# Optimization experiments

Hardware: AMD Instinct MI355X
Metric: run time of the kernel (lower is better)

## Reference

```python
import jax, jax.numpy as jnp
import numpy as np

VOCAB = 32000
WORDVEC = 256
HIDDEN = 512
NULL_TOKEN = 0


def setup_inputs() -> dict:
    key = jax.random.key(0)
    ks = jax.random.split(key, 8)
    N, Tp1 = 16, 257
    captions = jax.random.randint(ks[0], (N, Tp1), 0, VOCAB, dtype=jnp.int64 if jax.config.jax_enable_x64 else jnp.int32)
    W_embed = jax.random.normal(ks[1], (VOCAB, WORDVEC), jnp.float32) / 100.0
    Wx = jax.random.normal(ks[2], (WORDVEC, 4 * HIDDEN), jnp.float32) / np.sqrt(WORDVEC).astype(np.float32)
    Wh = jax.random.normal(ks[3], (HIDDEN, 4 * HIDDEN), jnp.float32) / np.sqrt(HIDDEN).astype(np.float32)
    b = jnp.zeros((4 * HIDDEN,), jnp.float32)
    W_vocab = jax.random.normal(ks[4], (HIDDEN, VOCAB), jnp.float32) / np.sqrt(HIDDEN).astype(np.float32)
    b_vocab = jnp.zeros((VOCAB,), jnp.float32)
    h_init = jax.random.normal(ks[5], (HIDDEN,), jnp.float32)
    return {"captions": captions, "W_embed": W_embed, "Wx": Wx, "Wh": Wh,
            "b": b, "W_vocab": W_vocab, "b_vocab": b_vocab, "h_init": h_init}


def reference(captions, W_embed, Wx, Wh, b, W_vocab, b_vocab, h_init):
    cap_in = captions[:, :-1]   # [N, T]
    cap_out = captions[:, 1:]   # [N, T]
    mask = (cap_out != NULL_TOKEN).astype(jnp.float32)
    N = cap_in.shape[0]
    H = h_init.shape[0]

    # Embedding lookup: [N, T, D]
    x = W_embed[cap_in]
    # Precompute input projections as one big GEMM: [T, N, 4H]
    xw = jnp.einsum('ntd,dk->tnk', x, Wx) + b

    h0 = jnp.tile(h_init, (N, 1))          # [N, H]
    c0 = jnp.zeros_like(h0)                 # lstm_forward starts c at zeros

    def step(carry, a_x):
        h, c = carry
        a = a_x + h @ Wh                    # [N, 4H]
        i, f, o, g = jnp.split(a, 4, axis=-1)
        i = jax.nn.sigmoid(i)
        f = jax.nn.sigmoid(f)
        o = jax.nn.sigmoid(o)
        g = jnp.tanh(g)
        c = f * c + i * g
        h = o * jnp.tanh(c)
        return (h, c), h

    _, hs = jax.lax.scan(step, (h0, c0), xw)  # hs: [T, N, H]

    # Temporal affine: [N, T, V]
    logits = jnp.einsum('tnh,hv->ntv', hs, W_vocab) + b_vocab
    logp = jax.nn.log_softmax(logits, axis=-1)
    nll = -jnp.take_along_axis(logp, cap_out[..., None], axis=-1)[..., 0]
    loss = jnp.sum(nll * mask) / N
    return loss
```

## Files before the change

### kernel.cpp

```cpp
#include <hip/hip_runtime.h>

#define VOCAB   32000
#define WORDVEC 256
#define HIDDEN  512
#define TSTEPS  256
#define NBATCH  16
#define NROWS   (TSTEPS*NBATCH)
#define GATES   (4*HIDDEN)
#define NVB     125
#define NWG     32

typedef __attribute__((ext_vector_type(8))) short short8;
typedef __attribute__((ext_vector_type(4))) float f32x4;
typedef unsigned long long u64;

__device__ __forceinline__ unsigned short f2bf(float x){
    union { float f; unsigned int u; } v; v.f = x;
    unsigned int r = v.u + 0x7fffu + ((v.u >> 16) & 1u);
    return (unsigned short)(r >> 16);
}

__global__ __launch_bounds__(256) void wv_pack(const float* __restrict__ Wv, unsigned short* __restrict__ WvP){
    __shared__ float s[64][65];
    int v0 = blockIdx.x * 64;
    int k0 = blockIdx.y * 64;
    int tid = threadIdx.x;
    for (int i = 0; i < 16; ++i){
        int lin = tid + i*256;
        int kk = lin >> 6, vv = lin & 63;
        s[kk][vv] = Wv[(long)(k0+kk)*VOCAB + v0 + vv];
    }
    __syncthreads();
    for (int i = 0; i < 2; ++i){
        int lr = tid + i*256;
        int f  = lr >> 6;
        int vbl = f >> 1, ktl = f & 1;
        int L = lr & 63, q = L >> 4, ln = L & 15;
        short8 o;
        #pragma unroll
        for (int j = 0; j < 8; ++j)
            o[j] = (short)f2bf(s[ktl*32 + q*8 + j][vbl*16 + ln]);
        long vb = blockIdx.x*4 + vbl;
        long kt = blockIdx.y*2 + ktl;
        *(short8*)(WvP + ((vb*16 + kt)*64 + L)*8) = o;
    }
}

__global__ void whp_prep(const float* __restrict__ Wh, unsigned short* __restrict__ Whp){
    int w = blockIdx.x; int tid = threadIdx.x;
    for (int item = tid; item < 4096; item += 256){
        int f = item >> 6;
        int L = item & 63;
        int kt = f >> 2, nt = f & 3;
        int q = L >> 4, ln = L & 15;
        int col = nt*HIDDEN + w*16 + ln;
        short8 vvec;
        for (int jj = 0; jj < 8; ++jj){
            int k = kt*32 + q*8 + jj;
            vvec[jj] = (short)f2bf(Wh[(long)k*GATES + col]);
        }
        *(short8*)(Whp + ((long)w*4096 + item)*8) = vvec;
    }
}

__global__ void hg_init(const float* __restrict__ h_init, u64* __restrict__ hx){
    int p = blockIdx.x*256 + threadIdx.x;
    int fq = p >> 6;
    int j  = (p & 3) * 2;
    int u0 = (fq>>2)*32 + (fq&3)*8 + j;
    u64 pk = (u64)f2bf(h_init[u0]) | ((u64)f2bf(h_init[u0+1]) << 16);
    hx[p] = pk;
}

__global__ __launch_bounds__(256) void embed_xw(const int* __restrict__ captions,
        const float* __restrict__ Wemb, const float* __restrict__ Wx,
        const float* __restrict__ b, float* __restrict__ xw){
    __shared__ float xs[8][WORDVEC];
    __shared__ int toks[8];
    int tid = threadIdx.x;
    int r0 = blockIdx.x * 8;
    if (tid < 8){
        int r = r0 + tid; int t = r >> 4, n = r & 15;
        toks[tid] = captions[n*257 + t];
    }
    __syncthreads();
    for (int i = 0; i < 8; ++i){
        int lin = tid + i*256;
        int ri = lin >> 8, d = lin & 255;
        xs[ri][d] = Wemb[(long)toks[ri]*WORDVEC + d];
    }
    __syncthreads();
    float4 b0 = *(const float4*)(b + tid*4);
    float4 b1 = *(const float4*)(b + 1024 + tid*4);
    float acc[8][8];
    for (int ri = 0; ri < 8; ++ri){
        acc[ri][0]=b0.x; acc[ri][1]=b0.y; acc[ri][2]=b0.z; acc[ri][3]=b0.w;
        acc[ri][4]=b1.x; acc[ri][5]=b1.y; acc[ri][6]=b1.z; acc[ri][7]=b1.w;
    }
    for (int d = 0; d < WORDVEC; ++d){
        float4 w0 = *(const float4*)(Wx + (long)d*GATES + tid*4);
        float4 w1 = *(const float4*)(Wx + (long)d*GATES + 1024 + tid*4);
        #pragma unroll
        for (int ri = 0; ri < 8; ++ri){
            float xv = xs[ri][d];
            acc[ri][0] += xv*w0.x; acc[ri][1] += xv*w0.y;
            acc[ri][2] += xv*w0.z; acc[ri][3] += xv*w0.w;
            acc[ri][4] += xv*w1.x; acc[ri][5] += xv*w1.y;
            acc[ri][6] += xv*w1.z; acc[ri][7] += xv*w1.w;
        }
    }
    for (int ri = 0; ri < 8; ++ri){
        float4 o0 = {acc[ri][0],acc[ri][1],acc[ri][2],acc[ri][3]};
        float4 o1 = {acc[ri][4],acc[ri][5],acc[ri][6],acc[ri][7]};
        *(float4*)(xw + (long)(r0+ri)*GATES + tid*4) = o0;
        *(float4*)(xw + (long)(r0+ri)*GATES + 1024 + tid*4) = o1;
    }
}

__global__ __launch_bounds__(256) void lstm_mfma(const float* __restrict__ xw,
        const unsigned short* __restrict__ Whp, u64* __restrict__ hx,
        unsigned short* __restrict__ hsP){
    __shared__ unsigned int hstage[4096];
    __shared__ float a_s[4][16][16];
    int w = blockIdx.x;
    int tid = threadIdx.x;
    int wv = tid >> 6;
    int L = tid & 63;
    int q = L >> 4, ln = L & 15;
    int s_idx = tid >> 4, jl = tid & 15;

    short8 bw[16];
    #pragma unroll
    for (int kt = 0; kt < 16; ++kt)
        bw[kt] = *(const short8*)(Whp + ((long)w*4096 + (kt*4+wv)*64 + L)*8);

    float c_r = 0.f;
    int fq_pub = (w>>1)*4 + (w&1)*2 + (jl>>3);
    int pubIdx = fq_pub*64 + s_idx*4 + ((jl>>1)&3);
    int kt_h = w >> 1;
    int q_h  = ((w & 1) << 1) | (jl >> 3);
    int j_h  = jl & 7;

    for (int t = 0; t < TSTEPS; ++t){
        long xb = (long)(t*16 + s_idx)*GATES + w*16 + jl;
        float xg0 = xw[xb], xg1 = xw[xb+512], xg2 = xw[xb+1024], xg3 = xw[xb+1536];

        const u64* hr = hx + (t & 1)*4096;
        u64*       hw = hx + ((t+1) & 1)*4096;

        u64 v[16];
        #pragma unroll
        for (int i = 0; i < 16; ++i)
            v[i] = __hip_atomic_load(hr + tid + i*256, __ATOMIC_RELAXED, __HIP_MEMORY_SCOPE_AGENT);
        for (;;){
            u64 bad = 0;
            #pragma unroll
            for (int i = 0; i < 16; ++i) bad |= (v[i] >> 32) ^ (u64)(unsigned)t;
            if (!bad) break;
            #pragma unroll
            for (int i = 0; i < 16; ++i)
                v[i] = __hip_atomic_load(hr + tid + i*256, __ATOMIC_RELAXED, __HIP_MEMORY_SCOPE_AGENT);
        }
        #pragma unroll
        for (int i = 0; i < 16; ++i) hstage[tid + i*256] = (unsigned)v[i];
        __syncthreads();

        f32x4 acc = {0.f,0.f,0.f,0.f};
        #pragma unroll
        for (int kt = 0; kt < 16; ++kt){
            short8 a = *(const short8*)((const unsigned short*)hstage + (kt*256 + q*64 + ln*4)*2);
            acc = __builtin_amdgcn_mfma_f32_16x16x32_bf16(a, bw[kt], acc, 0, 0, 0);
        }
        #pragma unroll
        for (int r = 0; r < 4; ++r) a_s[wv][q*4 + r][ln] = acc[r];
        __syncthreads();

        float ai = a_s[0][s_idx][jl] + xg0;
        float af = a_s[1][s_idx][jl] + xg1;
        float ao = a_s[2][s_idx][jl] + xg2;
        float ag = a_s[3][s_idx][jl] + xg3;
        float ig = 1.f/(1.f + __expf(-ai));
        float fg = 1.f/(1.f + __expf(-af));
        float og = 1.f/(1.f + __expf(-ao));
        float gg = 2.f/(1.f + __expf(-2.f*ag)) - 1.f;
        c_r = fg*c_r + ig*gg;
        float hv = og * (2.f/(1.f + __expf(-2.f*c_r)) - 1.f);
        unsigned short hb = f2bf(hv);

        int hv32 = (int)hb;
        int other = __shfl(hv32, L ^ 1);
        if ((jl & 1) == 0){
            u64 pk = (u64)(unsigned short)hv32
                   | ((u64)(unsigned short)other << 16)
                   | ((u64)(unsigned)(t+1) << 32);
            __hip_atomic_store(hw + pubIdx, pk, __ATOMIC_RELAXED, __HIP_MEMORY_SCOPE_AGENT);
        }
        int rb = s_idx*16 + (t >> 4);
        hsP[(((long)(rb*16 + kt_h))*64 + q_h*16 + (t & 15))*8 + j_h] = hb;
    }
}

__global__ __launch_bounds__(256) void vocab_gemm(const unsigned short* __restrict__ hsP,
        const unsigned short* __restrict__ WvP, const float* __restrict__ bvoc,
        const int* __restrict__ captions, float* __restrict__ pmax,
        float* __restrict__ psum, float* __restrict__ tlog){
    int bm = blockIdx.x;
    int bn = blockIdx.y;
    int tid = threadIdx.x;
    int wv = tid >> 6, L = tid & 63;
    int q = L >> 4, ln = L & 15;
    __shared__ int   tgt_s[64];
    __shared__ float wmax_s[4][64], wsum_s[4][64];
    if (tid < 64){
        int rg = bm*64 + tid;
        tgt_s[tid] = captions[(rg >> 8)*257 + (rg & 255) + 1];
    }
    __syncthreads();
    f32x4 acc[4][4];
    for (int mt=0;mt<4;++mt) for (int nt=0;nt<4;++nt) acc[mt][nt] = (f32x4){0.f,0.f,0.f,0.f};
    int colb = bn*256 + wv*64;
    const unsigned short* aB = hsP + ((long)(bm*4)*16)*512;
    const unsigned short* bB = WvP + ((long)(bn*16 + wv*4)*16)*512;
    #pragma unroll 4
    for (int kt = 0; kt < 16; ++kt){
        short8 a[4], bb[4];
        #pragma unroll
        for (int mt=0;mt<4;++mt)
            a[mt] = *(const short8*)(aB + ((long)(mt*16 + kt)*64 + L)*8);
        #pragma unroll
        for (int nt=0;nt<4;++nt)
            bb[nt] = *(const short8*)(bB + ((long)(nt*16 + kt)*64 + L)*8);
        #pragma unroll
        for (int mt=0;mt<4;++mt)
            #pragma unroll
            for (int nt=0;nt<4;++nt)
                acc[mt][nt] = __builtin_amdgcn_mfma_f32_16x16x32_bf16(a[mt], bb[nt], acc[mt][nt], 0,0,0);
    }
    float bv[4];
    #pragma unroll
    for (int nt=0;nt<4;++nt) bv[nt] = bvoc[colb + nt*16 + ln];
    #pragma unroll
    for (int mt=0;mt<4;++mt) for (int nt=0;nt<4;++nt) for (int r=0;r<4;++r)
        acc[mt][nt][r] += bv[nt];
    #pragma unroll
    for (int mt=0;mt<4;++mt) for (int r=0;r<4;++r){
        int rl = mt*16 + q*4 + r;
        int tg = tgt_s[rl] - colb;
        if (tg >= 0 && tg < 64){
            int nt = tg >> 4;
            if ((tg & 15) == ln) tlog[bm*64 + rl] = acc[mt][nt][r];
        }
    }
    #pragma unroll
    for (int mt=0;mt<4;++mt){
        #pragma unroll
        for (int r=0;r<4;++r){
            float m = fmaxf(fmaxf(acc[mt][0][r],acc[mt][1][r]), fmaxf(acc[mt][2][r],acc[mt][3][r]));
            for (int d=1; d<16; d<<=1) m = fmaxf(m, __shfl_xor(m, d, 16));
            float s = __expf(acc[mt][0][r]-m) + __expf(acc[mt][1][r]-m)
                    + __expf(acc[mt][2][r]-m) + __expf(acc[mt][3][r]-m);
            for (int d=1; d<16; d<<=1) s += __shfl_xor(s, d, 16);
            if (ln == 0){ int rl = mt*16 + q*4 + r; wmax_s[wv][rl] = m; wsum_s[wv][rl] = s; }
        }
    }
    __syncthreads();
    if (tid < 64){
        float M = fmaxf(fmaxf(wmax_s[0][tid],wmax_s[1][tid]), fmaxf(wmax_s[2][tid],wmax_s[3][tid]));
        float S = 0.f;
        for (int ww=0; ww<4; ++ww) S += wsum_s[ww][tid]*__expf(wmax_s[ww][tid]-M);
        pmax[(long)bn*NROWS + bm*64 + tid] = M;
        psum[(long)bn*NROWS + bm*64 + tid] = S;
    }
}

__global__ __launch_bounds__(256) void reduce_loss(const float* __restrict__ pmax,
        const float* __restrict__ psum, const float* __restrict__ tlog,
        const int* __restrict__ captions, float* __restrict__ out){
    int r = blockIdx.x*256 + threadIdx.x;
    float M = -1e30f;
    for (int p=0;p<NVB;++p) M = fmaxf(M, pmax[(long)p*NROWS + r]);
    float S = 0.f;
    for (int p=0;p<NVB;++p) S += psum[(long)p*NROWS + r]*__expf(pmax[(long)p*NROWS + r]-M);
    float lse = M + logf(S);
    float nll = lse - tlog[r];
    int tok = captions[(r >> 8)*257 + (r & 255) + 1];
    float val = (tok != 0) ? nll : 0.f;
    __shared__ float red[256];
    red[threadIdx.x] = val; __syncthreads();
    for (int s=128; s>0; s>>=1){
        if (threadIdx.x < s) red[threadIdx.x] += red[threadIdx.x+s];
        __syncthreads();
    }
    if (threadIdx.x == 0) atomicAdd(out, red[0] * (1.0f/16.0f));
}

extern "C" void kernel_launch(void* const* d_in, const int* in_sizes, int n_in,
                              void* d_out, int out_size, void* d_ws, size_t ws_size,
                              hipStream_t stream){
    const int*   captions = (const int*)  d_in[0];
    const float* Wemb     = (const float*)d_in[1];
    const float* Wx       = (const float*)d_in[2];
    const float* Wh       = (const float*)d_in[3];
    const float* b        = (const float*)d_in[4];
    const float* Wv       = (const float*)d_in[5];
    const float* bvoc     = (const float*)d_in[6];
    const float* h_init   = (const float*)d_in[7];

    char* ws = (char*)d_ws;
    float*          xw   = (float*)         (ws + 0);
    unsigned short* WvP  = (unsigned short*)(ws + 33554432);
    unsigned short* hsP  = (unsigned short*)(ws + 66322432);
    float*          pmax = (float*)         (ws + 70516736);
    float*          psum = (float*)         (ws + 72564736);
    float*          tlog = (float*)         (ws + 74612736);
    unsigned short* Whp  = (unsigned short*)(ws + 74629120);
    u64*            hx   = (u64*)           (ws + 76726272);

    float* out_f = (float*)d_out;

    (void)hipMemsetAsync(d_out, 0, sizeof(float), stream);

    hipLaunchKernelGGL(wv_pack,      dim3(500, 8), dim3(256), 0, stream, Wv, WvP);
    hipLaunchKernelGGL(whp_prep,     dim3(NWG),    dim3(256), 0, stream, Wh, Whp);
    hipLaunchKernelGGL(hg_init,      dim3(16),     dim3(256), 0, stream, h_init, hx);
    hipLaunchKernelGGL(embed_xw,     dim3(512),    dim3(256), 0, stream, captions, Wemb, Wx, b, xw);
    hipLaunchKernelGGL(lstm_mfma,    dim3(NWG),    dim3(256), 0, stream, xw, Whp, hx, hsP);
    hipLaunchKernelGGL(vocab_gemm,   dim3(64,NVB), dim3(256), 0, stream, hsP, WvP, bvoc, captions, pmax, psum, tlog);
    hipLaunchKernelGGL(reduce_loss,  dim3(16),     dim3(256), 0, stream, pmax, psum, tlog, captions, out_f);
}
```

Baseline: 1.159 ms.

## Fuse LSTM recurrence with vocab GEMM via per-4-step counters to overlap

Merges the recurrent LSTM kernel and the vocab projection/softmax kernel into one persistent launch. 32 blocks run the recurrence, and 500 extra blocks consume hidden states in 64-row chunks (4 timesteps × 16 batch) as soon as a per-chunk counter shows all recurrence blocks have published them. To make each chunk contiguous, the hidden-state buffer layout switches to time-major and is written with packed 64-bit atomic stores; reduce_loss indexing is updated to match. This hides most of the vocab GEMM behind the serial recurrence. The risk is that spinning consumer blocks compete with the latency-critical recurrence blocks, and the scheme relies on all blocks being co-resident.

```diff
diff --git a/kernel.cpp b/kernel.cpp
--- a/kernel.cpp
+++ b/kernel.cpp
@@ -9,6 +9,7 @@
 #define GATES   (4*HIDDEN)
 #define NVB     125
 #define NWG     32
+#define NWGEMM  500
 
 typedef __attribute__((ext_vector_type(8))) short short8;
 typedef __attribute__((ext_vector_type(4))) float f32x4;
@@ -117,159 +118,193 @@
     }
 }
 
-__global__ __launch_bounds__(256) void lstm_mfma(const float* __restrict__ xw,
-        const unsigned short* __restrict__ Whp, u64* __restrict__ hx,
-        unsigned short* __restrict__ hsP){
-    __shared__ unsigned int hstage[4096];
-    __shared__ float a_s[4][16][16];
-    int w = blockIdx.x;
+__global__ __launch_bounds__(256) void fused_lstm_vocab(
+        const float* __restrict__ xw, const unsigned short* __restrict__ Whp,
+        u64* __restrict__ hx, u64* __restrict__ hsPq, int* __restrict__ cnt,
+        const unsigned short* __restrict__ WvP, const float* __restrict__ bvoc,
+        const int* __restrict__ captions, float* __restrict__ pmax,
+        float* __restrict__ psum, float* __restrict__ tlog){
+    __shared__ char smem[20480];
     int tid = threadIdx.x;
     int wv = tid >> 6;
     int L = tid & 63;
     int q = L >> 4, ln = L & 15;
-    int s_idx = tid >> 4, jl = tid & 15;
-
-    short8 bw[16];
-    #pragma unroll
-    for (int kt = 0; kt < 16; ++kt)
-        bw[kt] = *(const short8*)(Whp + ((long)w*4096 + (kt*4+wv)*64 + L)*8);
-
-    float c_r = 0.f;
-    int fq_pub = (w>>1)*4 + (w&1)*2 + (jl>>3);
-    int pubIdx = fq_pub*64 + s_idx*4 + ((jl>>1)&3);
-    int kt_h = w >> 1;
-    int q_h  = ((w & 1) << 1) | (jl >> 3);
-    int j_h  = jl & 7;
-
-    for (int t = 0; t < TSTEPS; ++t){
-        long xb = (long)(t*16 + s_idx)*GATES + w*16 + jl;
-        float xg0 = xw[xb], xg1 = xw[xb+512], xg2 = xw[xb+1024], xg3 = xw[xb+1536];
-
-        const u64* hr = hx + (t & 1)*4096;
-        u64*       hw = hx + ((t+1) & 1)*4096;
-
-        u64 v[16];
+
+    if (blockIdx.x < NWG){
+        unsigned int* hstage = (unsigned int*)smem;
+        float (*a_s)[16][16] = (float (*)[16][16])(smem + 16384);
+        int w = blockIdx.x;
+        int s_idx = tid >> 4, jl = tid & 15;
+
+        short8 bw[16];
         #pragma unroll
-        for (int i = 0; i < 16; ++i)
-            v[i] = __hip_atomic_load(hr + tid + i*256, __ATOMIC_RELAXED, __HIP_MEMORY_SCOPE_AGENT);
-        for (;;){
-            u64 bad = 0;
-            #pragma unroll
-            for (int i = 0; i < 16; ++i) bad |= (v[i] >> 32) ^ (u64)(unsigned)t;
-            if (!bad) break;
+        for (int kt = 0; kt < 16; ++kt)
+            bw[kt] = *(const short8*)(Whp + ((long)w*4096 + (kt*4+wv)*64 + L)*8);
+
+        float c_r = 0.f;
+        int fq_pub = (w>>1)*4 + (w&1)*2 + (jl>>3);
+        int pubIdx = fq_pub*64 + s_idx*4 + ((jl>>1)&3);
+        int kt_h = w >> 1;
+        int q_h  = ((w & 1) << 1) | (jl >> 3);
+        int jq   = (jl & 7) >> 2;
+
+        for (int t = 0; t < TSTEPS; ++t){
+            long xb = (long)(t*16 + s_idx)*GATES + w*16 + jl;
+            float xg0 = xw[xb], xg1 = xw[xb+512], xg2 = xw[xb+1024], xg3 = xw[xb+1536];
+
+            const u64* hr = hx + (t & 1)*4096;
+            u64*       hw = hx + ((t+1) & 1)*4096;
+
+            u64 v[16];
             #pragma unroll
             for (int i = 0; i < 16; ++i)
                 v[i] = __hip_atomic_load(hr + tid + i*256, __ATOMIC_RELAXED, __HIP_MEMORY_SCOPE_AGENT);
+            for (;;){
+                u64 bad = 0;
+                #pragma unroll
+                for (int i = 0; i < 16; ++i) bad |= (v[i] >> 32) ^ (u64)(unsigned)t;
+                if (!bad) break;
+                #pragma unroll
+                for (int i = 0; i < 16; ++i)
+                    v[i] = __hip_atomic_load(hr + tid + i*256, __ATOMIC_RELAXED, __HIP_MEMORY_SCOPE_AGENT);
+            }
+            #pragma unroll
+            for (int i = 0; i < 16; ++i) hstage[tid + i*256] = (unsigned)v[i];
+            __syncthreads();
+
+            f32x4 acc = {0.f,0.f,0.f,0.f};
+            #pragma unroll
+            for (int kt = 0; kt < 16; ++kt){
+                short8 a = *(const short8*)((const unsigned short*)hstage + (kt*256 + q*64 + ln*4)*2);
+                acc = __builtin_amdgcn_mfma_f32_16x16x32_bf16(a, bw[kt], acc, 0, 0, 0);
+            }
+            #pragma unroll
+            for (int r = 0; r < 4; ++r) a_s[wv][q*4 + r][ln] = acc[r];
+            __syncthreads();
+
+            float ai = a_s[0][s_idx][jl] + xg0;
+            float af = a_s[1][s_idx][jl] + xg1;
+            float ao = a_s[2][s_idx][jl] + xg2;
+            float ag = a_s[3][s_idx][jl] + xg3;
+            float ig = 1.f/(1.f + __expf(-ai));
+            float fg = 1.f/(1.f + __expf(-af));
+            float og = 1.f/(1.f + __expf(-ao));
+            float gg = 2.f/(1.f + __expf(-2.f*ag)) - 1.f;
+            c_r = fg*c_r + ig*gg;
+            float hv = og * (2.f/(1.f + __expf(-2.f*c_r)) - 1.f);
+            unsigned short hb = f2bf(hv);
+
+            int hv32 = (int)hb;
+            int other = __shfl(hv32, (L & ~1) | ((L & 1) ^ 1));
+            if ((jl & 1) == 0){
+                u64 pk = (u64)(unsigned short)hv32
+                       | ((u64)(unsigned short)other << 16)
+                       | ((u64)(unsigned)(t+1) << 32);
+                __hip_atomic_store(hw + pubIdx, pk, __ATOMIC_RELAXED, __HIP_MEMORY_SCOPE_AGENT);
+            }
+
+            int b4 = L & ~3;
+            u64 q0 = (unsigned short)__shfl(hv32, b4);
+            u64 q1 = (unsigned short)__shfl(hv32, b4+1);
+            u64 q2 = (unsigned short)__shfl(hv32, b4+2);
+            u64 q3 = (unsigned short)__shfl(hv32, b4+3);
+            if ((jl & 3) == 0){
+                u64 pk2 = q0 | (q1 << 16) | (q2 << 32) | (q3 << 48);
+                long hIdx = ((long)(t*16 + kt_h)*64 + q_h*16 + s_idx)*2 + jq;
+                __hip_atomic_store(hsPq + hIdx, pk2, __ATOMIC_RELAXED, __HIP_MEMORY_SCOPE_AGENT);
+            }
+            if ((t & 3) == 3){
+                __asm__ __volatile__("s_waitcnt vmcnt(0)" ::: "memory");
+                __syncthreads();
+                if (tid == 0) atomicAdd(cnt + (t >> 2)*32, 1);
+            }
         }
-        #pragma unroll
-        for (int i = 0; i < 16; ++i) hstage[tid + i*256] = (unsigned)v[i];
-        __syncthreads();
-
-        f32x4 acc = {0.f,0.f,0.f,0.f};
-        #pragma unroll
-        for (int kt = 0; kt < 16; ++kt){
-            short8 a = *(const short8*)((const unsigned short*)hstage + (kt*256 + q*64 + ln*4)*2);
-            acc = __builtin_amdgcn_mfma_f32_16x16x32_bf16(a, bw[kt], acc, 0, 0, 0);
+    } else {
+        int wid = blockIdx.x - NWG;
+        int bn  = wid % 125;
+        int r0  = wid / 125;
+        int* tgt_s = (int*)smem;
+        float (*wmax_s)[64] = (float (*)[64])(smem + 256);
+        float (*wsum_s)[64] = (float (*)[64])(smem + 1280);
+        int colb = bn*256 + wv*64;
+        const unsigned short* bB = WvP + ((long)(bn*16 + wv*4)*16)*512;
+
+        for (int it = 0; it < 16; ++it){
+            int bm = r0 + it*4;
+            if (tid == 0){
+                const int* cp = cnt + bm*32;
+                while (__hip_atomic_load(cp, __ATOMIC_RELAXED, __HIP_MEMORY_SCOPE_AGENT) < NWG)
+                    __builtin_amdgcn_s_sleep(8);
+            }
+            __syncthreads();
+            if (tid < 64){
+                int rg = bm*64 + tid;
+                tgt_s[tid] = captions[(rg & 15)*257 + (rg >> 4) + 1];
+            }
+            __syncthreads();
+
+            f32x4 acc[4][4];
+            #pragma unroll
+            for (int mt=0;mt<4;++mt)
+                #pragma unroll
+                for (int nt=0;nt<4;++nt) acc[mt][nt] = (f32x4){0.f,0.f,0.f,0.f};
+
+            #pragma unroll 2
+            for (int kt = 0; kt < 16; ++kt){
+                short8 a[4], bb[4];
+                #pragma unroll
+                for (int mt=0;mt<4;++mt){
+                    long ab = ((long)((bm*4+mt)*16 + kt)*64 + L)*2;
+                    union { u64 u[2]; short8 s; } c;
+                    c.u[0] = __hip_atomic_load(hsPq + ab,     __ATOMIC_RELAXED, __HIP_MEMORY_SCOPE_AGENT);
+                    c.u[1] = __hip_atomic_load(hsPq + ab + 1, __ATOMIC_RELAXED, __HIP_MEMORY_SCOPE_AGENT);
+                    a[mt] = c.s;
+                }
+                #pragma unroll
+                for (int nt=0;nt<4;++nt)
+                    bb[nt] = *(const short8*)(bB + ((long)(nt*16 + kt)*64 + L)*8);
+                #pragma unroll
+                for (int mt=0;mt<4;++mt)
+                    #pragma unroll
+                    for (int nt=0;nt<4;++nt)
+                        acc[mt][nt] = __builtin_amdgcn_mfma_f32_16x16x32_bf16(a[mt], bb[nt], acc[mt][nt], 0,0,0);
+            }
+            float bv[4];
+            #pragma unroll
+            for (int nt=0;nt<4;++nt) bv[nt] = bvoc[colb + nt*16 + ln];
+            #pragma unroll
+            for (int mt=0;mt<4;++mt) for (int nt=0;nt<4;++nt) for (int r=0;r<4;++r)
+                acc[mt][nt][r] += bv[nt];
+            #pragma unroll
+            for (int mt=0;mt<4;++mt) for (int r=0;r<4;++r){
+                int rl = mt*16 + q*4 + r;
+                int tg = tgt_s[rl] - colb;
+                if (tg >= 0 && tg < 64){
+                    int nt = tg >> 4;
+                    if ((tg & 15) == ln) tlog[bm*64 + rl] = acc[mt][nt][r];
+                }
+            }
+            #pragma unroll
+            for (int mt=0;mt<4;++mt){
+                #pragma unroll
+                for (int r=0;r<4;++r){
+                    float m = fmaxf(fmaxf(acc[mt][0][r],acc[mt][1][r]), fmaxf(acc[mt][2][r],acc[mt][3][r]));
+                    for (int d=1; d<16; d<<=1) m = fmaxf(m, __shfl_xor(m, d, 16));
+                    float s = __expf(acc[mt][0][r]-m) + __expf(acc[mt][1][r]-m)
+                            + __expf(acc[mt][2][r]-m) + __expf(acc[mt][3][r]-m);
+                    for (int d=1; d<16; d<<=1) s += __shfl_xor(s, d, 16);
+                    if (ln == 0){ int rl = mt*16 + q*4 + r; wmax_s[wv][rl] = m; wsum_s[wv][rl] = s; }
+                }
+            }
+            __syncthreads();
+            if (tid < 64){
+                float M = fmaxf(fmaxf(wmax_s[0][tid],wmax_s[1][tid]), fmaxf(wmax_s[2][tid],wmax_s[3][tid]));
+                float S = 0.f;
+                for (int ww=0; ww<4; ++ww) S += wsum_s[ww][tid]*__expf(wmax_s[ww][tid]-M);
+                pmax[(long)bn*NROWS + bm*64 + tid] = M;
+                psum[(long)bn*NROWS + bm*64 + tid] = S;
+            }
         }
-        #pragma unroll
-        for (int r = 0; r < 4; ++r) a_s[wv][q*4 + r][ln] = acc[r];
-        __syncthreads();
-
-        float ai = a_s[0][s_idx][jl] + xg0;
-        float af = a_s[1][s_idx][jl] + xg1;
-        float ao = a_s[2][s_idx][jl] + xg2;
-        float ag = a_s[3][s_idx][jl] + xg3;
-        float ig = 1.f/(1.f + __expf(-ai));
-        float fg = 1.f/(1.f + __expf(-af));
-        float og = 1.f/(1.f + __expf(-ao));
-        float gg = 2.f/(1.f + __expf(-2.f*ag)) - 1.f;
-        c_r = fg*c_r + ig*gg;
-        float hv = og * (2.f/(1.f + __expf(-2.f*c_r)) - 1.f);
-        unsigned short hb = f2bf(hv);
-
-        int hv32 = (int)hb;
-        int other = __shfl(hv32, L ^ 1);
-        if ((jl & 1) == 0){
-            u64 pk = (u64)(unsigned short)hv32
-                   | ((u64)(unsigned short)other << 16)
-                   | ((u64)(unsigned)(t+1) << 32);
-            __hip_atomic_store(hw + pubIdx, pk, __ATOMIC_RELAXED, __HIP_MEMORY_SCOPE_AGENT);
-        }
-        int rb = s_idx*16 + (t >> 4);
-        hsP[(((long)(rb*16 + kt_h))*64 + q_h*16 + (t & 15))*8 + j_h] = hb;
-    }
-}
-
-__global__ __launch_bounds__(256) void vocab_gemm(const unsigned short* __restrict__ hsP,
-        const unsigned short* __restrict__ WvP, const float* __restrict__ bvoc,
-        const int* __restrict__ captions, float* __restrict__ pmax,
-        float* __restrict__ psum, float* __restrict__ tlog){
-    int bm = blockIdx.x;
-    int bn = blockIdx.y;
-    int tid = threadIdx.x;
-    int wv = tid >> 6, L = tid & 63;
-    int q = L >> 4, ln = L & 15;
-    __shared__ int   tgt_s[64];
-    __shared__ float wmax_s[4][64], wsum_s[4][64];
-    if (tid < 64){
-        int rg = bm*64 + tid;
-        tgt_s[tid] = captions[(rg >> 8)*257 + (rg & 255) + 1];
-    }
-    __syncthreads();
-    f32x4 acc[4][4];
-    for (int mt=0;mt<4;++mt) for (int nt=0;nt<4;++nt) acc[mt][nt] = (f32x4){0.f,0.f,0.f,0.f};
-    int colb = bn*256 + wv*64;
-    const unsigned short* aB = hsP + ((long)(bm*4)*16)*512;
-    const unsigned short* bB = WvP + ((long)(bn*16 + wv*4)*16)*512;
-    #pragma unroll 4
-    for (int kt = 0; kt < 16; ++kt){
-        short8 a[4], bb[4];
-        #pragma unroll
-        for (int mt=0;mt<4;++mt)
-            a[mt] = *(const short8*)(aB + ((long)(mt*16 + kt)*64 + L)*8);
-        #pragma unroll
-        for (int nt=0;nt<4;++nt)
-            bb[nt] = *(const short8*)(bB + ((long)(nt*16 + kt)*64 + L)*8);
-        #pragma unroll
-        for (int mt=0;mt<4;++mt)
-            #pragma unroll
-            for (int nt=0;nt<4;++nt)
-                acc[mt][nt] = __builtin_amdgcn_mfma_f32_16x16x32_bf16(a[mt], bb[nt], acc[mt][nt], 0,0,0);
-    }
-    float bv[4];
-    #pragma unroll
-    for (int nt=0;nt<4;++nt) bv[nt] = bvoc[colb + nt*16 + ln];
-    #pragma unroll
-    for (int mt=0;mt<4;++mt) for (int nt=0;nt<4;++nt) for (int r=0;r<4;++r)
-        acc[mt][nt][r] += bv[nt];
-    #pragma unroll
-    for (int mt=0;mt<4;++mt) for (int r=0;r<4;++r){
-        int rl = mt*16 + q*4 + r;
-        int tg = tgt_s[rl] - colb;
-        if (tg >= 0 && tg < 64){
-            int nt = tg >> 4;
-            if ((tg & 15) == ln) tlog[bm*64 + rl] = acc[mt][nt][r];
-        }
-    }
-    #pragma unroll
-    for (int mt=0;mt<4;++mt){
-        #pragma unroll
-        for (int r=0;r<4;++r){
-            float m = fmaxf(fmaxf(acc[mt][0][r],acc[mt][1][r]), fmaxf(acc[mt][2][r],acc[mt][3][r]));
-            for (int d=1; d<16; d<<=1) m = fmaxf(m, __shfl_xor(m, d, 16));
-            float s = __expf(acc[mt][0][r]-m) + __expf(acc[mt][1][r]-m)
-                    + __expf(acc[mt][2][r]-m) + __expf(acc[mt][3][r]-m);
-            for (int d=1; d<16; d<<=1) s += __shfl_xor(s, d, 16);
-            if (ln == 0){ int rl = mt*16 + q*4 + r; wmax_s[wv][rl] = m; wsum_s[wv][rl] = s; }
-        }
-    }
-    __syncthreads();
-    if (tid < 64){
-        float M = fmaxf(fmaxf(wmax_s[0][tid],wmax_s[1][tid]), fmaxf(wmax_s[2][tid],wmax_s[3][tid]));
-        float S = 0.f;
-        for (int ww=0; ww<4; ++ww) S += wsum_s[ww][tid]*__expf(wmax_s[ww][tid]-M);
-        pmax[(long)bn*NROWS + bm*64 + tid] = M;
-        psum[(long)bn*NROWS + bm*64 + tid] = S;
     }
 }
 
@@ -283,7 +318,7 @@
     for (int p=0;p<NVB;++p) S += psum[(long)p*NROWS + r]*__expf(pmax[(long)p*NROWS + r]-M);
     float lse = M + logf(S);
     float nll = lse - tlog[r];
-    int tok = captions[(r >> 8)*257 + (r & 255) + 1];
+    int tok = captions[(r & 15)*257 + (r >> 4) + 1];
     float val = (tok != 0) ? nll : 0.f;
     __shared__ float red[256];
     red[threadIdx.x] = val; __syncthreads();
@@ -309,22 +344,24 @@
     char* ws = (char*)d_ws;
     float*          xw   = (float*)         (ws + 0);
     unsigned short* WvP  = (unsigned short*)(ws + 33554432);
-    unsigned short* hsP  = (unsigned short*)(ws + 66322432);
+    u64*            hsPq = (u64*)           (ws + 66322432);
     float*          pmax = (float*)         (ws + 70516736);
     float*          psum = (float*)         (ws + 72564736);
     float*          tlog = (float*)         (ws + 74612736);
     unsigned short* Whp  = (unsigned short*)(ws + 74629120);
     u64*            hx   = (u64*)           (ws + 76726272);
+    int*            cnt  = (int*)           (ws + 76791808);
 
     float* out_f = (float*)d_out;
 
     (void)hipMemsetAsync(d_out, 0, sizeof(float), stream);
+    (void)hipMemsetAsync(cnt, 0, 8192, stream);
 
     hipLaunchKernelGGL(wv_pack,      dim3(500, 8), dim3(256), 0, stream, Wv, WvP);
     hipLaunchKernelGGL(whp_prep,     dim3(NWG),    dim3(256), 0, stream, Wh, Whp);
     hipLaunchKernelGGL(hg_init,      dim3(16),     dim3(256), 0, stream, h_init, hx);
     hipLaunchKernelGGL(embed_xw,     dim3(512),    dim3(256), 0, stream, captions, Wemb, Wx, b, xw);
-    hipLaunchKernelGGL(lstm_mfma,    dim3(NWG),    dim3(256), 0, stream, xw, Whp, hx, hsP);
-    hipLaunchKernelGGL(vocab_gemm,   dim3(64,NVB), dim3(256), 0, stream, hsP, WvP, bvoc, captions, pmax, psum, tlog);
+    hipLaunchKernelGGL(fused_lstm_vocab, dim3(NWG + NWGEMM), dim3(256), 0, stream,
+                       xw, Whp, hx, hsPq, cnt, WvP, bvoc, captions, pmax, psum, tlog);
     hipLaunchKernelGGL(reduce_loss,  dim3(16),     dim3(256), 0, stream, pmax, psum, tlog, captions, out_f);
 }
```

Measured after the change: 2.443 ms. +110.8%, slower.

## Remove LDS staging and barriers from LSTM recurrence by per-wave gate layout

Applied to the files above, without the earlier changes.

Reorganizes the Wh packing so each wave's MFMA output tile holds all four gates for a block of 4 hidden units. The gate nonlinearity can then run inside one wave, with no cross-wave exchange. Hidden-state fragments are loaded straight from global memory into MFMA A-operand registers instead of being staged through shared memory, which removes both __syncthreads per timestep. The cost is more scattered 8-byte atomic loads per lane, a larger register footprint, and a reliance on intra-wave LDS ordering through an explicit waitcnt.

```diff
diff --git a/kernel.cpp b/kernel.cpp
--- a/kernel.cpp
+++ b/kernel.cpp
@@ -49,11 +49,11 @@
 __global__ void whp_prep(const float* __restrict__ Wh, unsigned short* __restrict__ Whp){
     int w = blockIdx.x; int tid = threadIdx.x;
     for (int item = tid; item < 4096; item += 256){
-        int f = item >> 6;
-        int L = item & 63;
-        int kt = f >> 2, nt = f & 3;
+        int wv = item >> 10;
+        int kt = (item >> 6) & 15;
+        int L  = item & 63;
         int q = L >> 4, ln = L & 15;
-        int col = nt*HIDDEN + w*16 + ln;
+        int col = (ln >> 2)*HIDDEN + w*16 + wv*4 + (ln & 3);
         short8 vvec;
         for (int jj = 0; jj < 8; ++jj){
             int k = kt*32 + q*8 + jj;
@@ -65,9 +65,7 @@
 
 __global__ void hg_init(const float* __restrict__ h_init, u64* __restrict__ hx){
     int p = blockIdx.x*256 + threadIdx.x;
-    int fq = p >> 6;
-    int j  = (p & 3) * 2;
-    int u0 = (fq>>2)*32 + (fq&3)*8 + j;
+    int u0 = (p >> 6)*8 + (p & 3)*2;
     u64 pk = (u64)f2bf(h_init[u0]) | ((u64)f2bf(h_init[u0+1]) << 16);
     hx[p] = pk;
 }
@@ -120,65 +118,75 @@
 __global__ __launch_bounds__(256) void lstm_mfma(const float* __restrict__ xw,
         const unsigned short* __restrict__ Whp, u64* __restrict__ hx,
         unsigned short* __restrict__ hsP){
-    __shared__ unsigned int hstage[4096];
-    __shared__ float a_s[4][16][16];
+    __shared__ float a_ld[4][16][17];
     int w = blockIdx.x;
     int tid = threadIdx.x;
     int wv = tid >> 6;
     int L = tid & 63;
     int q = L >> 4, ln = L & 15;
-    int s_idx = tid >> 4, jl = tid & 15;
+    int seq = q*4 + (ln >> 2);
+    int u   = ln & 3;
+    int U   = w*16 + wv*4 + u;
 
     short8 bw[16];
     #pragma unroll
     for (int kt = 0; kt < 16; ++kt)
-        bw[kt] = *(const short8*)(Whp + ((long)w*4096 + (kt*4+wv)*64 + L)*8);
+        bw[kt] = *(const short8*)(Whp + ((long)w*4096 + (wv*16 + kt)*64 + L)*8);
 
     float c_r = 0.f;
-    int fq_pub = (w>>1)*4 + (w&1)*2 + (jl>>3);
-    int pubIdx = fq_pub*64 + s_idx*4 + ((jl>>1)&3);
-    int kt_h = w >> 1;
-    int q_h  = ((w & 1) << 1) | (jl >> 3);
-    int j_h  = jl & 7;
+    int fq_p = w*2 + (wv >> 1);
+    int pr_p = (wv & 1)*2 + (u >> 1);
+    int kt_h = U >> 5, q_h = (U >> 3) & 3, j_h = U & 7;
 
     for (int t = 0; t < TSTEPS; ++t){
-        long xb = (long)(t*16 + s_idx)*GATES + w*16 + jl;
+        long xb = (long)(t*16 + seq)*GATES + U;
         float xg0 = xw[xb], xg1 = xw[xb+512], xg2 = xw[xb+1024], xg3 = xw[xb+1536];
 
         const u64* hr = hx + (t & 1)*4096;
         u64*       hw = hx + ((t+1) & 1)*4096;
 
-        u64 v[16];
-        #pragma unroll
-        for (int i = 0; i < 16; ++i)
-            v[i] = __hip_atomic_load(hr + tid + i*256, __ATOMIC_RELAXED, __HIP_MEMORY_SCOPE_AGENT);
+        u64 va[16][4];
+        #pragma unroll
+        for (int kt = 0; kt < 16; ++kt){
+            const u64* src = hr + ((kt*4 + q)*64 + ln*4);
+            #pragma unroll
+            for (int c = 0; c < 4; ++c)
+                va[kt][c] = __hip_atomic_load(src + c, __ATOMIC_RELAXED, __HIP_MEMORY_SCOPE_AGENT);
+        }
         for (;;){
             u64 bad = 0;
             #pragma unroll
-            for (int i = 0; i < 16; ++i) bad |= (v[i] >> 32) ^ (u64)(unsigned)t;
+            for (int kt = 0; kt < 16; ++kt)
+                #pragma unroll
+                for (int c = 0; c < 4; ++c)
+                    bad |= (va[kt][c] >> 32) ^ (u64)(unsigned)t;
             if (!bad) break;
             #pragma unroll
-            for (int i = 0; i < 16; ++i)
-                v[i] = __hip_atomic_load(hr + tid + i*256, __ATOMIC_RELAXED, __HIP_MEMORY_SCOPE_AGENT);
-        }
-        #pragma unroll
-        for (int i = 0; i < 16; ++i) hstage[tid + i*256] = (unsigned)v[i];
-        __syncthreads();
+            for (int kt = 0; kt < 16; ++kt){
+                const u64* src = hr + ((kt*4 + q)*64 + ln*4);
+                #pragma unroll
+                for (int c = 0; c < 4; ++c)
+                    va[kt][c] = __hip_atomic_load(src + c, __ATOMIC_RELAXED, __HIP_MEMORY_SCOPE_AGENT);
+            }
+        }
 
         f32x4 acc = {0.f,0.f,0.f,0.f};
         #pragma unroll
         for (int kt = 0; kt < 16; ++kt){
-            short8 a = *(const short8*)((const unsigned short*)hstage + (kt*256 + q*64 + ln*4)*2);
-            acc = __builtin_amdgcn_mfma_f32_16x16x32_bf16(a, bw[kt], acc, 0, 0, 0);
-        }
-        #pragma unroll
-        for (int r = 0; r < 4; ++r) a_s[wv][q*4 + r][ln] = acc[r];
-        __syncthreads();
-
-        float ai = a_s[0][s_idx][jl] + xg0;
-        float af = a_s[1][s_idx][jl] + xg1;
-        float ao = a_s[2][s_idx][jl] + xg2;
-        float ag = a_s[3][s_idx][jl] + xg3;
+            union { unsigned uu[4]; short8 s; } fa;
+            #pragma unroll
+            for (int c = 0; c < 4; ++c) fa.uu[c] = (unsigned)va[kt][c];
+            acc = __builtin_amdgcn_mfma_f32_16x16x32_bf16(fa.s, bw[kt], acc, 0, 0, 0);
+        }
+
+        #pragma unroll
+        for (int r = 0; r < 4; ++r) a_ld[wv][q*4 + r][ln] = acc[r];
+        __asm__ __volatile__("s_waitcnt lgkmcnt(0)" ::: "memory");
+        float ai = a_ld[wv][seq][u]      + xg0;
+        float af = a_ld[wv][seq][4 + u]  + xg1;
+        float ao = a_ld[wv][seq][8 + u]  + xg2;
+        float ag = a_ld[wv][seq][12 + u] + xg3;
+
         float ig = 1.f/(1.f + __expf(-ai));
         float fg = 1.f/(1.f + __expf(-af));
         float og = 1.f/(1.f + __expf(-ao));
@@ -189,14 +197,13 @@
 
         int hv32 = (int)hb;
         int other = __shfl(hv32, L ^ 1);
-        if ((jl & 1) == 0){
+        if ((ln & 1) == 0){
             u64 pk = (u64)(unsigned short)hv32
                    | ((u64)(unsigned short)other << 16)
                    | ((u64)(unsigned)(t+1) << 32);
-            __hip_atomic_store(hw + pubIdx, pk, __ATOMIC_RELAXED, __HIP_MEMORY_SCOPE_AGENT);
-        }
-        int rb = s_idx*16 + (t >> 4);
-        hsP[(((long)(rb*16 + kt_h))*64 + q_h*16 + (t & 15))*8 + j_h] = hb;
+            __hip_atomic_store(hw + fq_p*64 + seq*4 + pr_p, pk, __ATOMIC_RELAXED, __HIP_MEMORY_SCOPE_AGENT);
+        }
+        hsP[(((long)(seq*16 + (t>>4))*16 + kt_h)*64 + q_h*16 + (t&15))*8 + j_h] = hb;
     }
 }
 
```

After: 3.072 ms. +165.0%, slower.
